# Performance work log

Hardware: AMD Instinct MI355X
Metric: run time of the kernel (lower is better)

The kernel has to match this reference:

```python
import jax, jax.numpy as jnp
import numpy as np

N_NODES = 50000
N_EDGES = 800000
D = 128


def setup_inputs() -> dict:
    key = jax.random.key(0)
    ks = jax.random.split(key, 6)
    stdv = 1.0 / np.sqrt(D)
    inputs = {
        "input": jax.random.normal(ks[0], (N_NODES, D), dtype=jnp.float32),
        "h0": jax.random.normal(ks[1], (N_NODES, D), dtype=jnp.float32),
        # COO representation of the (normalized) sparse adjacency
        "vals": jax.random.uniform(ks[2], (N_EDGES,), dtype=jnp.float32) / 16.0,
        "weight": jax.random.uniform(ks[3], (D, D), dtype=jnp.float32, minval=-stdv, maxval=stdv),
        "lamda": jnp.float32(0.5),
        "alpha": jnp.float32(0.1),
        "row": jax.random.randint(ks[4], (N_EDGES,), 0, N_NODES),
        "col": jax.random.randint(ks[5], (N_EDGES,), 0, N_NODES),
        "l": 4,
    }
    return inputs


def reference(input, h0, vals, weight, lamda, alpha, row, col, l):
    # theta = log(lamda / l + 1)
    theta = jnp.log(lamda / l + 1.0)
    # hi = spmm(adj, input): gather source-node features, scale by edge
    # values, scatter-add into destination rows.  [E, D] -> [N, D]
    hi = jax.ops.segment_sum(vals[:, None] * input[col], row, num_segments=input.shape[0])
    # variant=False path
    support = (1.0 - alpha) * hi + alpha * h0
    r = support
    # output = theta * support @ W + (1 - theta) * r
    output = theta * jnp.matmul(support, weight) + (1.0 - theta) * r
    return output
```

## Files before the change

kernel.cpp:

```cpp
#include <hip/hip_runtime.h>
#include <cmath>

constexpr int N_NODES = 50000;
constexpr int N_EDGES = 800000;
constexpr int D = 128;
constexpr int CAP = 32;
constexpr int OVF_CAP = 8192;

constexpr int NPART = 8;
constexpr int ROWS_PER_PART = (N_NODES + NPART - 1) / NPART;
constexpr int EPB = 8192;
constexpr int BPP = (N_EDGES + EPB - 1) / EPB;
constexpr int SCAT_BLOCKS = NPART * BPP;
constexpr int CAST_BLOCKS = (N_NODES * D / 8 + 255) / 256;

constexpr size_t OFF_OVFCNT = 200000;
constexpr size_t OFF_BUCKET = 200064;
constexpr size_t OFF_OVF    = 6600064;
constexpr size_t OFF_PACKED = 6731136;
constexpr size_t OFF_WT     = 19531136;

typedef __attribute__((ext_vector_type(8))) short bf16x8;
typedef __attribute__((ext_vector_type(4))) float f32x4;

__device__ __forceinline__ unsigned bf16rn(float f) {
    unsigned u = __float_as_uint(f);
    return (u + 0x7fffu + ((u >> 16) & 1u)) >> 16;
}
__device__ __forceinline__ float bf_lo(unsigned u) { return __uint_as_float(u << 16); }
__device__ __forceinline__ float bf_hi(unsigned u) { return __uint_as_float(u & 0xffff0000u); }

__device__ __forceinline__ unsigned enc_val(float v) {
    int m = (int)(v * 1048576.0f + 0.5f);
    if (m > 65535) m = 65535;
    if (m < 0) m = 0;
    return (unsigned)m;
}

__global__ __launch_bounds__(256) void scatter_cast(
    const int* __restrict__ row, const int* __restrict__ col,
    const float* __restrict__ vals, const float* __restrict__ input,
    const float* __restrict__ weight,
    int* __restrict__ cnt, unsigned* __restrict__ bucket,
    int* __restrict__ ovf_cnt, int4* __restrict__ ovf,
    unsigned* __restrict__ packed, ushort* __restrict__ wt)
{
    if (blockIdx.x < SCAT_BLOCKS) {
        const int p  = blockIdx.x & (NPART - 1);
        const int cb = blockIdx.x / NPART;
        const int lo = p * ROWS_PER_PART;
        const int hi = lo + ROWS_PER_PART;
        const int gbase = cb * (EPB / 4);

        #pragma unroll
        for (int it = 0; it < EPB / 4 / 256; ++it) {
            int gi = gbase + it * 256 + threadIdx.x;
            if (gi >= N_EDGES / 4) break;
            int4 r4 = ((const int4*)row)[gi];
            int e = gi * 4;
            int r;
            r = r4.x;
            if (r >= lo && r < hi) {
                unsigned ent = (unsigned)col[e] | (enc_val(vals[e]) << 16);
                int pos = atomicAdd(&cnt[r], 1);
                if (pos < CAP) bucket[(size_t)r * CAP + pos] = ent;
                else { int o = atomicAdd(ovf_cnt, 1);
                       if (o < OVF_CAP) ovf[o] = make_int4(r, (int)(ent & 0xffffu),
                           __float_as_int((float)(ent >> 16) * (1.0f / 1048576.0f)), 0); }
            }
            r = r4.y;
            if (r >= lo && r < hi) {
                unsigned ent = (unsigned)col[e + 1] | (enc_val(vals[e + 1]) << 16);
                int pos = atomicAdd(&cnt[r], 1);
                if (pos < CAP) bucket[(size_t)r * CAP + pos] = ent;
                else { int o = atomicAdd(ovf_cnt, 1);
                       if (o < OVF_CAP) ovf[o] = make_int4(r, (int)(ent & 0xffffu),
                           __float_as_int((float)(ent >> 16) * (1.0f / 1048576.0f)), 0); }
            }
            r = r4.z;
            if (r >= lo && r < hi) {
                unsigned ent = (unsigned)col[e + 2] | (enc_val(vals[e + 2]) << 16);
                int pos = atomicAdd(&cnt[r], 1);
                if (pos < CAP) bucket[(size_t)r * CAP + pos] = ent;
                else { int o = atomicAdd(ovf_cnt, 1);
                       if (o < OVF_CAP) ovf[o] = make_int4(r, (int)(ent & 0xffffu),
                           __float_as_int((float)(ent >> 16) * (1.0f / 1048576.0f)), 0); }
            }
            r = r4.w;
            if (r >= lo && r < hi) {
                unsigned ent = (unsigned)col[e + 3] | (enc_val(vals[e + 3]) << 16);
                int pos = atomicAdd(&cnt[r], 1);
                if (pos < CAP) bucket[(size_t)r * CAP + pos] = ent;
                else { int o = atomicAdd(ovf_cnt, 1);
                       if (o < OVF_CAP) ovf[o] = make_int4(r, (int)(ent & 0xffffu),
                           __float_as_int((float)(ent >> 16) * (1.0f / 1048576.0f)), 0); }
            }
        }
    } else if (blockIdx.x < SCAT_BLOCKS + CAST_BLOCKS) {
        int i = (blockIdx.x - SCAT_BLOCKS) * 256 + threadIdx.x;
        if (i >= N_NODES * D / 8) return;
        const float4* f = (const float4*)(input + (size_t)i * 8);
        float4 a = f[0], b = f[1];
        uint4 o;
        o.x = bf16rn(a.x) | (bf16rn(a.y) << 16);
        o.y = bf16rn(a.z) | (bf16rn(a.w) << 16);
        o.z = bf16rn(b.x) | (bf16rn(b.y) << 16);
        o.w = bf16rn(b.z) | (bf16rn(b.w) << 16);
        ((uint4*)packed)[i] = o;
    } else {
        #pragma unroll
        for (int j = 0; j < 64; ++j) {
            int idx = threadIdx.x + j * 256;
            int k = idx >> 7, n = idx & 127;
            wt[n * 128 + k] = (ushort)bf16rn(weight[idx]);
        }
    }
}

__global__ __launch_bounds__(256) void gather_support(
    const unsigned* __restrict__ packed,
    const float* __restrict__ h0,
    const float* __restrict__ alpha_p,
    const int* __restrict__ cnt,
    const unsigned* __restrict__ bucket,
    float* __restrict__ support)
{
    const float alpha = *alpha_p;
    const float oma = 1.0f - alpha;
    const int wv   = threadIdx.x >> 6;
    const int lane = threadIdx.x & 63;
    const int q    = lane & 15;
    const int slot = lane >> 4;

    const int g = blockIdx.x * 4 + wv;
    if (g >= N_NODES) return;

    int n = cnt[g];
    if (n > CAP) n = CAP;
    const unsigned* b = bucket + (size_t)g * CAP;
    const uint4* pk = (const uint4*)packed;

    const int q4 = (n + 3) >> 2;
    const int s0 = slot * q4;
    int s1 = s0 + q4; if (s1 > n) s1 = n;

    float acc[8] = {0.f, 0.f, 0.f, 0.f, 0.f, 0.f, 0.f, 0.f};
    for (int e = s0; e < s1; e += 4) {
        int rem = s1 - e;
        unsigned m0 = b[e];
        unsigned m1 = (rem > 1) ? b[e + 1] : 0u;
        unsigned m2 = (rem > 2) ? b[e + 2] : 0u;
        unsigned m3 = (rem > 3) ? b[e + 3] : 0u;
        uint4 x0 = pk[(size_t)(m0 & 0xffffu) * 16 + q];
        uint4 x1 = pk[(size_t)(m1 & 0xffffu) * 16 + q];
        uint4 x2 = pk[(size_t)(m2 & 0xffffu) * 16 + q];
        uint4 x3 = pk[(size_t)(m3 & 0xffffu) * 16 + q];
        float v0 = (float)(m0 >> 16) * (1.0f / 1048576.0f);
        float v1 = (float)(m1 >> 16) * (1.0f / 1048576.0f);
        float v2 = (float)(m2 >> 16) * (1.0f / 1048576.0f);
        float v3 = (float)(m3 >> 16) * (1.0f / 1048576.0f);
        acc[0] += v0 * bf_lo(x0.x); acc[1] += v0 * bf_hi(x0.x);
        acc[2] += v0 * bf_lo(x0.y); acc[3] += v0 * bf_hi(x0.y);
        acc[4] += v0 * bf_lo(x0.z); acc[5] += v0 * bf_hi(x0.z);
        acc[6] += v0 * bf_lo(x0.w); acc[7] += v0 * bf_hi(x0.w);
        acc[0] += v1 * bf_lo(x1.x); acc[1] += v1 * bf_hi(x1.x);
        acc[2] += v1 * bf_lo(x1.y); acc[3] += v1 * bf_hi(x1.y);
        acc[4] += v1 * bf_lo(x1.z); acc[5] += v1 * bf_hi(x1.z);
        acc[6] += v1 * bf_lo(x1.w); acc[7] += v1 * bf_hi(x1.w);
        acc[0] += v2 * bf_lo(x2.x); acc[1] += v2 * bf_hi(x2.x);
        acc[2] += v2 * bf_lo(x2.y); acc[3] += v2 * bf_hi(x2.y);
        acc[4] += v2 * bf_lo(x2.z); acc[5] += v2 * bf_hi(x2.z);
        acc[6] += v2 * bf_lo(x2.w); acc[7] += v2 * bf_hi(x2.w);
        acc[0] += v3 * bf_lo(x3.x); acc[1] += v3 * bf_hi(x3.x);
        acc[2] += v3 * bf_lo(x3.y); acc[3] += v3 * bf_hi(x3.y);
        acc[4] += v3 * bf_lo(x3.z); acc[5] += v3 * bf_hi(x3.z);
        acc[6] += v3 * bf_lo(x3.w); acc[7] += v3 * bf_hi(x3.w);
    }
    #pragma unroll
    for (int j = 0; j < 8; ++j) {
        acc[j] += __shfl_xor(acc[j], 16);
        acc[j] += __shfl_xor(acc[j], 32);
    }
    if (slot == 0) {
        const float* hp = h0 + (size_t)g * D + q * 8;
        float4 ha = *(const float4*)(hp);
        float4 hb = *(const float4*)(hp + 4);
        float* sp = support + (size_t)g * D + q * 8;
        float4 sa, sb;
        sa.x = oma * acc[0] + alpha * ha.x;
        sa.y = oma * acc[1] + alpha * ha.y;
        sa.z = oma * acc[2] + alpha * ha.z;
        sa.w = oma * acc[3] + alpha * ha.w;
        sb.x = oma * acc[4] + alpha * hb.x;
        sb.y = oma * acc[5] + alpha * hb.y;
        sb.z = oma * acc[6] + alpha * hb.z;
        sb.w = oma * acc[7] + alpha * hb.w;
        *(float4*)(sp) = sa;
        *(float4*)(sp + 4) = sb;
    }
}

__global__ __launch_bounds__(256) void ovf_apply(
    const float* __restrict__ input,
    const float* __restrict__ alpha_p,
    const int* __restrict__ ovf_cnt,
    const int4* __restrict__ ovf,
    float* __restrict__ support)
{
    int n = *ovf_cnt;
    if (n > OVF_CAP) n = OVF_CAP;
    const float oma = 1.0f - *alpha_p;
    for (int i = blockIdx.x * 256 + threadIdx.x; i < n * 2; i += gridDim.x * 256) {
        int idx = i >> 1, part = i & 1;
        int4 m = ovf[idx];
        float v = oma * __int_as_float(m.z);
        const float* x = input + (size_t)m.y * D + part * 64;
        float* s = support + (size_t)m.x * D + part * 64;
        for (int k = 0; k < 64; ++k) atomicAdd(&s[k], v * x[k]);
    }
}

__global__ __launch_bounds__(256) void gemm_mfma(
    const ushort* __restrict__ wt,
    const float* __restrict__ lamda_p,
    const int* __restrict__ l_p,
    float* __restrict__ data)
{
    constexpr int SP = 136;
    __shared__ ushort sA[64 * SP];
    __shared__ ushort sB[128 * SP];

    const int tid = threadIdx.x;
    const float lamda = *lamda_p;
    const float theta = logf(lamda / (float)(*l_p) + 1.0f);
    const float omt = 1.0f - theta;
    const int row0 = blockIdx.x * 64;

    #pragma unroll
    for (int j = 0; j < 8; ++j) {
        int idx = j * 256 + tid;
        int n  = idx >> 4;
        int k8 = (idx & 15) << 3;
        *(uint4*)(&sB[n * SP + k8]) = ((const uint4*)wt)[idx];
    }
    #pragma unroll
    for (int j = 0; j < 8; ++j) {
        int idx = j * 256 + tid;
        int rr = idx >> 5;
        int c4 = (idx & 31) << 2;
        int g = row0 + rr;
        float4 s = make_float4(0.f, 0.f, 0.f, 0.f);
        if (g < N_NODES) s = *(const float4*)(data + (size_t)g * D + c4);
        uint2 pkv;
        pkv.x = bf16rn(s.x) | (bf16rn(s.y) << 16);
        pkv.y = bf16rn(s.z) | (bf16rn(s.w) << 16);
        *(uint2*)(&sA[rr * SP + c4]) = pkv;
    }
    __syncthreads();

    const int wave = tid >> 6;
    const int lane = tid & 63;
    const int m    = lane & 15;
    const int quad = lane >> 4;
    const int arow = wave * 16 + m;

    f32x4 acc[8] = {};
    #pragma unroll
    for (int kb = 0; kb < 4; ++kb) {
        bf16x8 a = *(const bf16x8*)(&sA[arow * SP + kb * 32 + quad * 8]);
        #pragma unroll
        for (int nt = 0; nt < 8; ++nt) {
            bf16x8 b = *(const bf16x8*)(&sB[(nt * 16 + m) * SP + kb * 32 + quad * 8]);
            acc[nt] = __builtin_amdgcn_mfma_f32_16x16x32_bf16(a, b, acc[nt], 0, 0, 0);
        }
    }

    const int gbase = row0 + wave * 16 + quad * 4;
    #pragma unroll
    for (int nt = 0; nt < 8; ++nt) {
        int colb = nt * 16 + m;
        #pragma unroll
        for (int i = 0; i < 4; ++i) {
            int g = gbase + i;
            if (g < N_NODES) {
                size_t off = (size_t)g * D + colb;
                float s = data[off];
                data[off] = theta * acc[nt][i] + omt * s;
            }
        }
    }
}

extern "C" void kernel_launch(void* const* d_in, const int* in_sizes, int n_in,
                              void* d_out, int out_size, void* d_ws, size_t ws_size,
                              hipStream_t stream) {
    const float* input  = (const float*)d_in[0];
    const float* h0     = (const float*)d_in[1];
    const float* vals   = (const float*)d_in[2];
    const float* weight = (const float*)d_in[3];
    const float* lamda  = (const float*)d_in[4];
    const float* alpha  = (const float*)d_in[5];
    const int*   row    = (const int*)d_in[6];
    const int*   col    = (const int*)d_in[7];
    const int*   l      = (const int*)d_in[8];
    float* out = (float*)d_out;

    char* ws = (char*)d_ws;
    int*      cnt     = (int*)ws;
    int*      ovf_cnt = (int*)(ws + OFF_OVFCNT);
    unsigned* bucket  = (unsigned*)(ws + OFF_BUCKET);
    int4*     ovf     = (int4*)(ws + OFF_OVF);
    unsigned* packed  = (unsigned*)(ws + OFF_PACKED);
    ushort*   wt      = (ushort*)(ws + OFF_WT);

    hipMemsetAsync(ws, 0, OFF_BUCKET, stream);

    scatter_cast<<<SCAT_BLOCKS + CAST_BLOCKS + 1, 256, 0, stream>>>(
        row, col, vals, input, weight, cnt, bucket, ovf_cnt, ovf, packed, wt);

    int gatherb = (N_NODES + 3) / 4;
    gather_support<<<gatherb, 256, 0, stream>>>(packed, h0, alpha, cnt, bucket, out);

    ovf_apply<<<8, 256, 0, stream>>>(input, alpha, ovf_cnt, ovf, out);

    int gemmb = (N_NODES + 63) / 64;
    gemm_mfma<<<gemmb, 256, 0, stream>>>(wt, lamda, l, out);
}
```

Before: 208.9 us.

## Drop row-partitioned scatter passes and vectorize edge loads

Removes the 8-way destination-row partitioning in the bucket scatter, so each edge is read and pushed once instead of the row array being scanned by 8 partition passes. Column and value arrays are now loaded as int4/float4 vectors alongside rows, and the per-edge push logic is factored into a helper. This trades the cache locality of partitioned atomic writes into cnt and bucket for far less redundant index traffic and fewer blocks.

```diff
diff --git a/kernel.cpp b/kernel.cpp
--- a/kernel.cpp
+++ b/kernel.cpp
@@ -7,11 +7,8 @@
 constexpr int CAP = 32;
 constexpr int OVF_CAP = 8192;
 
-constexpr int NPART = 8;
-constexpr int ROWS_PER_PART = (N_NODES + NPART - 1) / NPART;
-constexpr int EPB = 8192;
-constexpr int BPP = (N_EDGES + EPB - 1) / EPB;
-constexpr int SCAT_BLOCKS = NPART * BPP;
+constexpr int EPB = 2048;
+constexpr int SCAT_BLOCKS = (N_EDGES + EPB - 1) / EPB;
 constexpr int CAST_BLOCKS = (N_NODES * D / 8 + 255) / 256;
 
 constexpr size_t OFF_OVFCNT = 200000;
@@ -35,6 +32,21 @@
     if (m > 65535) m = 65535;
     if (m < 0) m = 0;
     return (unsigned)m;
+}
+
+__device__ __forceinline__ void push_edge(
+    int r, int c, float v,
+    int* __restrict__ cnt, unsigned* __restrict__ bucket,
+    int* __restrict__ ovf_cnt, int4* __restrict__ ovf)
+{
+    unsigned ent = (unsigned)c | (enc_val(v) << 16);
+    int pos = atomicAdd(&cnt[r], 1);
+    if (pos < CAP) bucket[(size_t)r * CAP + pos] = ent;
+    else {
+        int o = atomicAdd(ovf_cnt, 1);
+        if (o < OVF_CAP) ovf[o] = make_int4(r, c,
+            __float_as_int((float)(ent >> 16) * (1.0f / 1048576.0f)), 0);
+    }
 }
 
 __global__ __launch_bounds__(256) void scatter_cast(
@@ -46,55 +58,19 @@
     unsigned* __restrict__ packed, ushort* __restrict__ wt)
 {
     if (blockIdx.x < SCAT_BLOCKS) {
-        const int p  = blockIdx.x & (NPART - 1);
-        const int cb = blockIdx.x / NPART;
-        const int lo = p * ROWS_PER_PART;
-        const int hi = lo + ROWS_PER_PART;
-        const int gbase = cb * (EPB / 4);
+        const int gbase = blockIdx.x * (EPB / 4);
 
         #pragma unroll
         for (int it = 0; it < EPB / 4 / 256; ++it) {
             int gi = gbase + it * 256 + threadIdx.x;
             if (gi >= N_EDGES / 4) break;
-            int4 r4 = ((const int4*)row)[gi];
-            int e = gi * 4;
-            int r;
-            r = r4.x;
-            if (r >= lo && r < hi) {
-                unsigned ent = (unsigned)col[e] | (enc_val(vals[e]) << 16);
-                int pos = atomicAdd(&cnt[r], 1);
-                if (pos < CAP) bucket[(size_t)r * CAP + pos] = ent;
-                else { int o = atomicAdd(ovf_cnt, 1);
-                       if (o < OVF_CAP) ovf[o] = make_int4(r, (int)(ent & 0xffffu),
-                           __float_as_int((float)(ent >> 16) * (1.0f / 1048576.0f)), 0); }
-            }
-            r = r4.y;
-            if (r >= lo && r < hi) {
-                unsigned ent = (unsigned)col[e + 1] | (enc_val(vals[e + 1]) << 16);
-                int pos = atomicAdd(&cnt[r], 1);
-                if (pos < CAP) bucket[(size_t)r * CAP + pos] = ent;
-                else { int o = atomicAdd(ovf_cnt, 1);
-                       if (o < OVF_CAP) ovf[o] = make_int4(r, (int)(ent & 0xffffu),
-                           __float_as_int((float)(ent >> 16) * (1.0f / 1048576.0f)), 0); }
-            }
-            r = r4.z;
-            if (r >= lo && r < hi) {
-                unsigned ent = (unsigned)col[e + 2] | (enc_val(vals[e + 2]) << 16);
-                int pos = atomicAdd(&cnt[r], 1);
-                if (pos < CAP) bucket[(size_t)r * CAP + pos] = ent;
-                else { int o = atomicAdd(ovf_cnt, 1);
-                       if (o < OVF_CAP) ovf[o] = make_int4(r, (int)(ent & 0xffffu),
-                           __float_as_int((float)(ent >> 16) * (1.0f / 1048576.0f)), 0); }
-            }
-            r = r4.w;
-            if (r >= lo && r < hi) {
-                unsigned ent = (unsigned)col[e + 3] | (enc_val(vals[e + 3]) << 16);
-                int pos = atomicAdd(&cnt[r], 1);
-                if (pos < CAP) bucket[(size_t)r * CAP + pos] = ent;
-                else { int o = atomicAdd(ovf_cnt, 1);
-                       if (o < OVF_CAP) ovf[o] = make_int4(r, (int)(ent & 0xffffu),
-                           __float_as_int((float)(ent >> 16) * (1.0f / 1048576.0f)), 0); }
-            }
+            int4   r4 = ((const int4*)row)[gi];
+            int4   c4 = ((const int4*)col)[gi];
+            float4 v4 = ((const float4*)vals)[gi];
+            push_edge(r4.x, c4.x, v4.x, cnt, bucket, ovf_cnt, ovf);
+            push_edge(r4.y, c4.y, v4.y, cnt, bucket, ovf_cnt, ovf);
+            push_edge(r4.z, c4.z, v4.z, cnt, bucket, ovf_cnt, ovf);
+            push_edge(r4.w, c4.w, v4.w, cnt, bucket, ovf_cnt, ovf);
         }
     } else if (blockIdx.x < SCAT_BLOCKS + CAST_BLOCKS) {
         int i = (blockIdx.x - SCAT_BLOCKS) * 256 + threadIdx.x;
```

Result: faster. 203.5 us (-2.6%).
